# Kernel optimization log

Hardware: AMD Instinct MI355X
Metric: run time of the kernel (lower is better)

## Reference

```python
import jax, jax.numpy as jnp
import numpy as np


def setup_inputs() -> dict:
    key = jax.random.key(0)
    ks = jax.random.split(key, 8)
    B, N, D, H = 8, 512, 64, 64
    user_embeddings = jax.random.normal(ks[0], (B, N, D), dtype=jnp.float32)
    past_lengths = jax.random.randint(ks[1], (B,), 0, N)
    valid_mask = jnp.ones((B, N), dtype=jnp.float32)
    # MLP params: Linear(4D -> H), PReLU (single slope), Linear(H -> 1)
    s1 = 1.0 / np.sqrt(4 * D)
    s2 = 1.0 / np.sqrt(H)
    W1 = jax.random.uniform(ks[2], (H, 4 * D), minval=-s1, maxval=s1, dtype=jnp.float32)
    b1 = jax.random.uniform(ks[3], (H,), minval=-s1, maxval=s1, dtype=jnp.float32)
    prelu_a = jnp.float32(0.25)
    W2 = jax.random.uniform(ks[4], (1, H), minval=-s2, maxval=s2, dtype=jnp.float32)
    b2 = jax.random.uniform(ks[5], (1,), minval=-s2, maxval=s2, dtype=jnp.float32)
    return {"past_lengths": past_lengths, "user_embeddings": user_embeddings,
            "valid_mask": valid_mask, "W1": W1, "b1": b1, "prelu_a": prelu_a,
            "W2": W2, "b2": b2}


def reference(past_lengths, user_embeddings, valid_mask, W1, b1, prelu_a, W2, b2):
    # DIN local activation attention with causal mask.
    # Original math: h = W1 @ concat(Q, K, Q-K, Q*K) + b1 per (q,k) pair.
    # Split W1 into its 4 D-sized blocks so the concat tensor [B,N,N,4D] is
    # never materialized; the pairwise hidden [B,N,N,H] is the only big buffer.
    B, N, D = user_embeddings.shape
    Wq, Wk, Wd, Wm = jnp.split(W1, 4, axis=1)  # each [H, D]
    x = user_embeddings
    # Q and (Q-K)'s +Q part -> per-query term; K and (Q-K)'s -K part -> per-key term
    hq = jnp.einsum('bqd,hd->bqh', x, Wq + Wd)          # [B,N,H]
    hk = jnp.einsum('bkd,hd->bkh', x, Wk - Wd)          # [B,N,H]
    hm = jnp.einsum('bqd,bkd,hd->bqkh', x, x, Wm)       # [B,N,N,H] (Q*K term)
    h = hq[:, :, None, :] + hk[:, None, :, :] + hm + b1
    h = jnp.where(h > 0, h, prelu_a * h)                # PReLU
    scores = jnp.einsum('bqkh,h->bqk', h, W2[0]) + b2[0]  # [B,N,N]
    causal = jnp.tril(jnp.ones((N, N), dtype=scores.dtype))
    scores = scores * causal[None, :, :]
    scores = scores * valid_mask[:, None, :]            # key-side padding mask
    encoded = jnp.einsum('bqk,bkd->bqd', scores, x)     # weighted sum (no softmax)
    return encoded
```

## Files before the change

kernel.cpp:

```cpp
#include <hip/hip_runtime.h>

#define NB 8
#define NN 512

#define WS_WMF 0
#define WS_HQ  4096
#define WS_BF  266240
#define WS_XE  528384

typedef float fx4 __attribute__((ext_vector_type(4)));
typedef short sx8 __attribute__((ext_vector_type(8)));
typedef int   ix4 __attribute__((ext_vector_type(4)));

static __device__ inline unsigned short f2bf(float f) {
    unsigned u = __float_as_uint(f);
    return (unsigned short)((u + 0x7FFFu + ((u >> 16) & 1u)) >> 16);
}

static __device__ inline void async_cp16(const void* g, void* l) {
    __builtin_amdgcn_global_load_lds(
        (const __attribute__((address_space(1))) unsigned int*)g,
        (__attribute__((address_space(3))) unsigned int*)l, 16, 0, 0);
}

__global__ __launch_bounds__(256) void prep(const float* __restrict__ x,
                                            const float* __restrict__ vm,
                                            const float* __restrict__ W1,
                                            const float* __restrict__ b1,
                                            float* __restrict__ ws) {
    __shared__ float lwq[64 * 68];
    __shared__ float lwk[64 * 68];
    __shared__ float xs[256];
    const int t = threadIdx.x;
    const int blk = blockIdx.x;

    {
        int d = t & 63, hb = t >> 6;
        #pragma unroll 4
        for (int i = 0; i < 16; ++i) {
            int h = i * 4 + hb;
            float a = W1[h * 256 + d];
            float bb = W1[h * 256 + 64 + d];
            float c = W1[h * 256 + 128 + d];
            lwq[h * 68 + d] = a + c;
            lwk[h * 68 + d] = bb - c;
        }
    }
    const int r0 = blk * 4;
    xs[t] = x[r0 * 64 + t];
    __syncthreads();

    {
        int r = t >> 6, h = t & 63;
        const fx4* xr  = (const fx4*)(xs + r * 64);
        const fx4* wqv = (const fx4*)(lwq + h * 68);
        const fx4* wkv = (const fx4*)(lwk + h * 68);
        float aq = b1[h], ak = 0.f;
        #pragma unroll
        for (int dd = 0; dd < 16; ++dd) {
            fx4 xv = xr[dd];
            fx4 wq = wqv[dd];
            fx4 wk = wkv[dd];
            aq = fmaf(xv[0], wq[0], aq); aq = fmaf(xv[1], wq[1], aq);
            aq = fmaf(xv[2], wq[2], aq); aq = fmaf(xv[3], wq[3], aq);
            ak = fmaf(xv[0], wk[0], ak); ak = fmaf(xv[1], wk[1], ak);
            ak = fmaf(xv[2], wk[2], ak); ak = fmaf(xv[3], wk[3], ak);
        }
        int row = r0 + r;
        (ws + WS_HQ)[row * 64 + h] = aq;
        unsigned short* bfp = (unsigned short*)(ws + WS_BF);
        int bb = row >> 9, k = row & 511;
        int tt = k >> 4, nn = k & 15;
        int c = 2 + (h >> 5);
        int qd = (h >> 3) & 3, j = h & 7;
        int ln = qd * 16 + nn;
        bfp[((((bb * 32 + tt) * 4 + c) * 64 + ln) << 3) + j] = f2bf(ak);
    }

    if (blk < 256) {
        int b = blk >> 5, t5 = blk & 31;
        if (t < 128) {
            unsigned short* bfp = (unsigned short*)(ws + WS_BF);
            int c = t >> 6, L = t & 63;
            int nn = L & 15, qd = L >> 4;
            const float* src = x + ((b * 512 + t5 * 16 + nn) * 64 + c * 32 + qd * 8);
            fx4 v0 = *(const fx4*)src;
            fx4 v1 = *(const fx4*)(src + 4);
            uint4 o;
            o.x = (unsigned)f2bf(v0[0]) | ((unsigned)f2bf(v0[1]) << 16);
            o.y = (unsigned)f2bf(v0[2]) | ((unsigned)f2bf(v0[3]) << 16);
            o.z = (unsigned)f2bf(v1[0]) | ((unsigned)f2bf(v1[1]) << 16);
            o.w = (unsigned)f2bf(v1[2]) | ((unsigned)f2bf(v1[3]) << 16);
            *(uint4*)(bfp + ((((b * 32 + t5) * 4 + c) * 64 + L) << 3)) = o;
        }
        {
            unsigned short* xep = (unsigned short*)(ws + WS_XE);
            int c32 = t5 >> 1, half = t5 & 1;
            int nt = t >> 6, r = t & 63;
            int L = half * 32 + (r & 31);
            int j0 = (r >> 5) * 4;
            int quad = L >> 4, nn = L & 15;
            unsigned short u[4];
            #pragma unroll
            for (int i = 0; i < 4; ++i) {
                int key = c32 * 32 + quad * 8 + j0 + i;
                float v = x[(b * 512 + key) * 64 + nt * 16 + nn] * vm[b * 512 + key];
                u[i] = f2bf(v);
            }
            uint2 o;
            o.x = (unsigned)u[0] | ((unsigned)u[1] << 16);
            o.y = (unsigned)u[2] | ((unsigned)u[3] << 16);
            *(uint2*)(xep + (((((b * 16 + c32) * 4 + nt) * 64 + L) << 3) + j0)) = o;
        }
    } else if (blk < 258) {
        float* wmf = ws + WS_WMF;
        int e = (blk - 256) * 256 + t;
        int slot = e >> 6, lane = e & 63;
        int ht = slot >> 1, hf = slot & 1;
        int mm = lane & 15, qd = lane >> 4;
        int h = ht * 16 + mm;
        int dbase = hf * 32 + qd * 8;
        #pragma unroll
        for (int j = 0; j < 8; ++j)
            wmf[e * 8 + j] = W1[h * 256 + 192 + dbase + j];
    }
}

__global__ __launch_bounds__(256, 2) void k2_main(const float* __restrict__ x,
                                                  const float* __restrict__ prelu_a,
                                                  const float* __restrict__ W2,
                                                  const float* __restrict__ b2,
                                                  const float* __restrict__ ws,
                                                  float* __restrict__ out) {
    const int tid  = threadIdx.x;
    const int lane = tid & 63;
    const int w    = tid >> 6;
    const int blk  = blockIdx.x;
    const int band = (int)((0x4501763298DCABEFULL >> ((blk >> 6) << 2)) & 0xF);
    const int rest = blk & 63;
    const int b    = rest >> 3;
    const int s    = rest & 7;
    const int n    = lane & 15, quad = lane >> 4;
    const int q    = band * 32 + s * 4 + w;
    const int bq   = b * 512 + q;
    const int cmax = band;

    const float* wmf = ws + WS_WMF;
    const float* hq  = ws + WS_HQ;
    const unsigned short* bfp = (const unsigned short*)(ws + WS_BF);
    const unsigned short* xep = (const unsigned short*)(ws + WS_XE);

    const float pa  = prelu_a[0];
    const float b2v = b2[0];

    __shared__ uint4 bufS[2][512];
    __shared__ uint4 bufE[2][256];
    __shared__ unsigned strip[4][16];

    fx4 w2v[4];
    #pragma unroll
    for (int ht = 0; ht < 4; ++ht)
        w2v[ht] = *(const fx4*)(W2 + ht * 16 + quad * 4);
    sx8 oh[4];
    #pragma unroll
    for (int ht = 0; ht < 4; ++ht) {
        sx8 a;
        #pragma unroll
        for (int jj = 0; jj < 8; ++jj) {
            int hp = (ht >> 1) * 32 + quad * 8 + jj;
            a[jj] = (hp == ht * 16 + n) ? (short)0x3F80 : (short)0;
        }
        oh[ht] = a;
    }
    const unsigned sel = (quad < 2) ? 0x05040100u : 0x07060302u;

    fx4 hqv[4];
    #pragma unroll
    for (int ht = 0; ht < 4; ++ht)
        hqv[ht] = *(const fx4*)(hq + bq * 64 + ht * 16 + quad * 4);
    float xq[2][8];
    {
        const float* xp = x + bq * 64 + quad * 8;
        fx4 t0 = *(const fx4*)xp;
        fx4 t1 = *(const fx4*)(xp + 4);
        fx4 t2 = *(const fx4*)(xp + 32);
        fx4 t3 = *(const fx4*)(xp + 36);
        #pragma unroll
        for (int jj = 0; jj < 4; ++jj) {
            xq[0][jj] = t0[jj]; xq[0][4 + jj] = t1[jj];
            xq[1][jj] = t2[jj]; xq[1][4 + jj] = t3[jj];
        }
    }
    sx8 afrag[4][2];
    #pragma unroll
    for (int ht = 0; ht < 4; ++ht)
        #pragma unroll
        for (int hf = 0; hf < 2; ++hf) {
            const float* wp = wmf + (((ht * 2 + hf) * 64 + lane) << 3);
            fx4 w0 = *(const fx4*)wp;
            fx4 w1 = *(const fx4*)(wp + 4);
            sx8 a;
            #pragma unroll
            for (int jj = 0; jj < 4; ++jj) {
                a[jj]     = (short)f2bf(w0[jj] * xq[hf][jj]);
                a[4 + jj] = (short)f2bf(w1[jj] * xq[hf][4 + jj]);
            }
            afrag[ht][hf] = a;
        }

    fx4 eacc[4];
    #pragma unroll
    for (int nt = 0; nt < 4; ++nt) eacc[nt] = (fx4){0.f, 0.f, 0.f, 0.f};

    {
        const uint4* sS = (const uint4*)(bfp + (unsigned)(b * 32) * 2048);
        const uint4* sE = (const uint4*)(xep + (unsigned)(b * 16) * 2048);
        async_cp16(sS + tid,       &bufS[0][tid]);
        async_cp16(sS + tid + 256, &bufS[0][tid + 256]);
        async_cp16(sE + tid,       &bufE[0][tid]);
    }
    __syncthreads();

    #pragma unroll 1
    for (int c = 0; c <= cmax; ++c) {
        if (c < cmax) {
            const int p2 = (c + 1) & 1;
            const uint4* sS = (const uint4*)(bfp + (unsigned)(b * 32 + 2 * (c + 1)) * 2048);
            const uint4* sE = (const uint4*)(xep + (unsigned)(b * 16 + c + 1) * 2048);
            async_cp16(sS + tid,       &bufS[p2][tid]);
            async_cp16(sS + tid + 256, &bufS[p2][tid + 256]);
            async_cp16(sE + tid,       &bufE[p2][tid]);
        }

        const int p = c & 1;
        const unsigned short* ls = (const unsigned short*)&bufS[p][0] + lane * 8;
        sx8 fa0 = *(const sx8*)(ls);
        sx8 fa1 = *(const sx8*)(ls + 512);
        sx8 fa2 = *(const sx8*)(ls + 1024);
        sx8 fa3 = *(const sx8*)(ls + 1536);
        sx8 fb0 = *(const sx8*)(ls + 2048);
        sx8 fb1 = *(const sx8*)(ls + 2560);
        sx8 fb2 = *(const sx8*)(ls + 3072);
        sx8 fb3 = *(const sx8*)(ls + 3584);

        fx4 accA[4], accB[4];
        #pragma unroll
        for (int ht = 0; ht < 4; ++ht) { accA[ht] = hqv[ht]; accB[ht] = hqv[ht]; }
        #pragma unroll
        for (int ht = 0; ht < 4; ++ht) {
            accA[ht] = __builtin_amdgcn_mfma_f32_16x16x32_bf16(afrag[ht][0], fa0, accA[ht], 0, 0, 0);
            accB[ht] = __builtin_amdgcn_mfma_f32_16x16x32_bf16(afrag[ht][0], fb0, accB[ht], 0, 0, 0);
        }
        #pragma unroll
        for (int ht = 0; ht < 4; ++ht) {
            accA[ht] = __builtin_amdgcn_mfma_f32_16x16x32_bf16(afrag[ht][1], fa1, accA[ht], 0, 0, 0);
            accB[ht] = __builtin_amdgcn_mfma_f32_16x16x32_bf16(afrag[ht][1], fb1, accB[ht], 0, 0, 0);
        }
        #pragma unroll
        for (int ht = 0; ht < 4; ++ht) {
            accA[ht] = __builtin_amdgcn_mfma_f32_16x16x32_bf16(oh[ht], (ht < 2) ? fa2 : fa3, accA[ht], 0, 0, 0);
            accB[ht] = __builtin_amdgcn_mfma_f32_16x16x32_bf16(oh[ht], (ht < 2) ? fb2 : fb3, accB[ht], 0, 0, 0);
        }

        fx4 s0v = (fx4){0.f, 0.f, 0.f, 0.f};
        fx4 s1v = (fx4){0.f, 0.f, 0.f, 0.f};
        #pragma unroll
        for (int ht = 0; ht < 4; ++ht) {
            fx4 za = accA[ht], zb = accB[ht];
            fx4 ta = __builtin_elementwise_max(za, za * pa);
            fx4 tb = __builtin_elementwise_max(zb, zb * pa);
            s0v = ta * w2v[ht] + s0v;
            s1v = tb * w2v[ht] + s1v;
        }
        float s0 = (s0v[0] + s0v[1]) + (s0v[2] + s0v[3]);
        float s1 = (s1v[0] + s1v[1]) + (s1v[2] + s1v[3]);
        s0 += __shfl_xor(s0, 16, 64);
        s0 += __shfl_xor(s0, 32, 64);
        s1 += __shfl_xor(s1, 16, 64);
        s1 += __shfl_xor(s1, 32, 64);
        int k0 = c * 32 + n;
        s0 = (k0 <= q)      ? s0 + b2v : 0.f;
        s1 = (k0 + 16 <= q) ? s1 + b2v : 0.f;

        unsigned packed = (unsigned)f2bf(s0) | ((unsigned)f2bf(s1) << 16);
        if (quad == 0) strip[w][n] = packed;
        const unsigned* sp = &strip[w][(quad & 1) * 8];
        uint4 wv0 = *(const uint4*)sp;
        uint4 wv1 = *(const uint4*)(sp + 4);
        ix4 sw_;
        sw_[0] = (int)__builtin_amdgcn_perm(wv0.y, wv0.x, sel);
        sw_[1] = (int)__builtin_amdgcn_perm(wv0.w, wv0.z, sel);
        sw_[2] = (int)__builtin_amdgcn_perm(wv1.y, wv1.x, sel);
        sw_[3] = (int)__builtin_amdgcn_perm(wv1.w, wv1.z, sel);
        sx8 sfrag = __builtin_bit_cast(sx8, sw_);

        const unsigned short* le = (const unsigned short*)&bufE[p][0] + lane * 8;
        sx8 e0 = *(const sx8*)(le);
        sx8 e1 = *(const sx8*)(le + 512);
        sx8 e2 = *(const sx8*)(le + 1024);
        sx8 e3 = *(const sx8*)(le + 1536);

        eacc[0] = __builtin_amdgcn_mfma_f32_16x16x32_bf16(sfrag, e0, eacc[0], 0, 0, 0);
        eacc[1] = __builtin_amdgcn_mfma_f32_16x16x32_bf16(sfrag, e1, eacc[1], 0, 0, 0);
        eacc[2] = __builtin_amdgcn_mfma_f32_16x16x32_bf16(sfrag, e2, eacc[2], 0, 0, 0);
        eacc[3] = __builtin_amdgcn_mfma_f32_16x16x32_bf16(sfrag, e3, eacc[3], 0, 0, 0);

        __syncthreads();
    }

    float ov = eacc[0][0];
    if (quad == 1) ov = eacc[1][0];
    if (quad == 2) ov = eacc[2][0];
    if (quad == 3) ov = eacc[3][0];
    out[bq * 64 + lane] = ov;
}

extern "C" void kernel_launch(void* const* d_in, const int* in_sizes, int n_in,
                              void* d_out, int out_size, void* d_ws, size_t ws_size,
                              hipStream_t stream) {
    const float* x   = (const float*)d_in[1];
    const float* vmk = (const float*)d_in[2];
    const float* W1  = (const float*)d_in[3];
    const float* b1  = (const float*)d_in[4];
    const float* pa  = (const float*)d_in[5];
    const float* W2  = (const float*)d_in[6];
    const float* b2  = (const float*)d_in[7];
    float* ws  = (float*)d_ws;
    float* out = (float*)d_out;

    hipLaunchKernelGGL(prep, dim3(NB * NN / 4), dim3(256), 0, stream,
                       x, vmk, W1, b1, ws);
    hipLaunchKernelGGL(k2_main, dim3(1024), dim3(256), 0, stream,
                       x, pa, W2, b2, ws, out);
}
```

Baseline: 98.04 us.

## Split prep into weight-prep and MFMA-based per-row projection kernels

The single prep kernel, where every one of 1024 blocks reloaded and combined the W1 blocks and computed the hq/hk projections with scalar FMAs, is replaced by two kernels. prepW builds the combined Wq+Wd and Wk-Wd matrices once in bf16 MFMA fragment layout, plus the Wm fragments. prepX uses 64 blocks that compute hq and hk with bf16 MFMA and also emit the bf16 x and masked-x layouts. This removes redundant weight loading and scalar dot products, but adds a kernel launch and lowers hq precision to bf16 inputs with far fewer blocks.

```diff
diff --git a/kernel.cpp b/kernel.cpp
--- a/kernel.cpp
+++ b/kernel.cpp
@@ -7,6 +7,7 @@
 #define WS_HQ  4096
 #define WS_BF  266240
 #define WS_XE  528384
+#define WS_WQF 659456
 
 typedef float fx4 __attribute__((ext_vector_type(4)));
 typedef short sx8 __attribute__((ext_vector_type(8)));
@@ -23,106 +24,133 @@
         (__attribute__((address_space(3))) unsigned int*)l, 16, 0, 0);
 }
 
-__global__ __launch_bounds__(256) void prep(const float* __restrict__ x,
-                                            const float* __restrict__ vm,
-                                            const float* __restrict__ W1,
-                                            const float* __restrict__ b1,
-                                            float* __restrict__ ws) {
-    __shared__ float lwq[64 * 68];
-    __shared__ float lwk[64 * 68];
-    __shared__ float xs[256];
-    const int t = threadIdx.x;
-    const int blk = blockIdx.x;
+__global__ __launch_bounds__(256) void prepW(const float* __restrict__ W1,
+                                             float* __restrict__ ws) {
+    const int t = threadIdx.x, blk = blockIdx.x;
+    unsigned short* wqf = (unsigned short*)(ws + WS_WQF);
 
     {
-        int d = t & 63, hb = t >> 6;
-        #pragma unroll 4
-        for (int i = 0; i < 16; ++i) {
-            int h = i * 4 + hb;
-            float a = W1[h * 256 + d];
-            float bb = W1[h * 256 + 64 + d];
-            float c = W1[h * 256 + 128 + d];
-            lwq[h * 68 + d] = a + c;
-            lwk[h * 68 + d] = bb - c;
-        }
-    }
-    const int r0 = blk * 4;
-    xs[t] = x[r0 * 64 + t];
-    __syncthreads();
-
-    {
-        int r = t >> 6, h = t & 63;
-        const fx4* xr  = (const fx4*)(xs + r * 64);
-        const fx4* wqv = (const fx4*)(lwq + h * 68);
-        const fx4* wkv = (const fx4*)(lwk + h * 68);
-        float aq = b1[h], ak = 0.f;
-        #pragma unroll
-        for (int dd = 0; dd < 16; ++dd) {
-            fx4 xv = xr[dd];
-            fx4 wq = wqv[dd];
-            fx4 wk = wkv[dd];
-            aq = fmaf(xv[0], wq[0], aq); aq = fmaf(xv[1], wq[1], aq);
-            aq = fmaf(xv[2], wq[2], aq); aq = fmaf(xv[3], wq[3], aq);
-            ak = fmaf(xv[0], wk[0], ak); ak = fmaf(xv[1], wk[1], ak);
-            ak = fmaf(xv[2], wk[2], ak); ak = fmaf(xv[3], wk[3], ak);
-        }
-        int row = r0 + r;
-        (ws + WS_HQ)[row * 64 + h] = aq;
-        unsigned short* bfp = (unsigned short*)(ws + WS_BF);
-        int bb = row >> 9, k = row & 511;
-        int tt = k >> 4, nn = k & 15;
-        int c = 2 + (h >> 5);
-        int qd = (h >> 3) & 3, j = h & 7;
-        int ln = qd * 16 + nn;
-        bfp[((((bb * 32 + tt) * 4 + c) * 64 + ln) << 3) + j] = f2bf(ak);
-    }
-
-    if (blk < 256) {
-        int b = blk >> 5, t5 = blk & 31;
-        if (t < 128) {
-            unsigned short* bfp = (unsigned short*)(ws + WS_BF);
-            int c = t >> 6, L = t & 63;
-            int nn = L & 15, qd = L >> 4;
-            const float* src = x + ((b * 512 + t5 * 16 + nn) * 64 + c * 32 + qd * 8);
-            fx4 v0 = *(const fx4*)src;
-            fx4 v1 = *(const fx4*)(src + 4);
-            uint4 o;
-            o.x = (unsigned)f2bf(v0[0]) | ((unsigned)f2bf(v0[1]) << 16);
-            o.y = (unsigned)f2bf(v0[2]) | ((unsigned)f2bf(v0[3]) << 16);
-            o.z = (unsigned)f2bf(v1[0]) | ((unsigned)f2bf(v1[1]) << 16);
-            o.w = (unsigned)f2bf(v1[2]) | ((unsigned)f2bf(v1[3]) << 16);
-            *(uint4*)(bfp + ((((b * 32 + t5) * 4 + c) * 64 + L) << 3)) = o;
-        }
-        {
-            unsigned short* xep = (unsigned short*)(ws + WS_XE);
-            int c32 = t5 >> 1, half = t5 & 1;
-            int nt = t >> 6, r = t & 63;
-            int L = half * 32 + (r & 31);
-            int j0 = (r >> 5) * 4;
-            int quad = L >> 4, nn = L & 15;
-            unsigned short u[4];
-            #pragma unroll
-            for (int i = 0; i < 4; ++i) {
-                int key = c32 * 32 + quad * 8 + j0 + i;
-                float v = x[(b * 512 + key) * 64 + nt * 16 + nn] * vm[b * 512 + key];
-                u[i] = f2bf(v);
-            }
-            uint2 o;
-            o.x = (unsigned)u[0] | ((unsigned)u[1] << 16);
-            o.y = (unsigned)u[2] | ((unsigned)u[3] << 16);
-            *(uint2*)(xep + (((((b * 16 + c32) * 4 + nt) * 64 + L) << 3) + j0)) = o;
-        }
-    } else if (blk < 258) {
+        int e = blk * 256 + t;
+        int slot = e >> 6, lane = e & 63;
+        int isK = slot >> 3, ht = (slot >> 1) & 3, half = slot & 1;
+        int n = lane & 15, qd = lane >> 4;
+        int h = ht * 16 + n, dbase = half * 32 + qd * 8;
+        unsigned short u[8];
+        #pragma unroll
+        for (int j = 0; j < 8; ++j) {
+            int d = dbase + j;
+            float wq = W1[h * 256 + d];
+            float wk = W1[h * 256 + 64 + d];
+            float wd = W1[h * 256 + 128 + d];
+            u[j] = f2bf(isK ? (wk - wd) : (wq + wd));
+        }
+        uint4 o;
+        o.x = (unsigned)u[0] | ((unsigned)u[1] << 16);
+        o.y = (unsigned)u[2] | ((unsigned)u[3] << 16);
+        o.z = (unsigned)u[4] | ((unsigned)u[5] << 16);
+        o.w = (unsigned)u[6] | ((unsigned)u[7] << 16);
+        ((uint4*)wqf)[e] = o;
+    }
+
+    if (blk < 2) {
         float* wmf = ws + WS_WMF;
-        int e = (blk - 256) * 256 + t;
+        int e = blk * 256 + t;
         int slot = e >> 6, lane = e & 63;
         int ht = slot >> 1, hf = slot & 1;
-        int mm = lane & 15, qd = lane >> 4;
-        int h = ht * 16 + mm;
+        int m = lane & 15, qd = lane >> 4;
+        int h = ht * 16 + m;
         int dbase = hf * 32 + qd * 8;
         #pragma unroll
         for (int j = 0; j < 8; ++j)
             wmf[e * 8 + j] = W1[h * 256 + 192 + dbase + j];
+    }
+}
+
+__global__ __launch_bounds__(256) void prepX(const float* __restrict__ x,
+                                             const float* __restrict__ vm,
+                                             const float* __restrict__ b1,
+                                             float* __restrict__ ws) {
+    const int t = threadIdx.x;
+    const int w = t >> 6, lane = t & 63;
+    const int n = lane & 15, quad = lane >> 4;
+    const int blk = blockIdx.x;
+    const int b   = blk >> 3;
+    const int tb  = (blk & 7) * 4;
+    const int tile = tb + w;
+
+    const unsigned short* wqf = (const unsigned short*)(ws + WS_WQF);
+    unsigned short* bfp = (unsigned short*)(ws + WS_BF);
+    unsigned short* xep = (unsigned short*)(ws + WS_XE);
+    float* hqp = ws + WS_HQ;
+
+    sx8 ax0, ax1;
+    {
+        const float* xp = x + ((b * 512 + tile * 16 + n) * 64 + quad * 8);
+        fx4 a0 = *(const fx4*)xp;
+        fx4 a1 = *(const fx4*)(xp + 4);
+        fx4 a2 = *(const fx4*)(xp + 32);
+        fx4 a3 = *(const fx4*)(xp + 36);
+        #pragma unroll
+        for (int j = 0; j < 4; ++j) {
+            ax0[j] = (short)f2bf(a0[j]); ax0[4 + j] = (short)f2bf(a1[j]);
+            ax1[j] = (short)f2bf(a2[j]); ax1[4 + j] = (short)f2bf(a3[j]);
+        }
+    }
+
+    *(uint4*)(bfp + ((((b * 32 + tile) * 4 + 0) * 64 + lane) << 3)) =
+        __builtin_bit_cast(uint4, ax0);
+    *(uint4*)(bfp + ((((b * 32 + tile) * 4 + 1) * 64 + lane) << 3)) =
+        __builtin_bit_cast(uint4, ax1);
+
+    #pragma unroll
+    for (int ht = 0; ht < 4; ++ht) {
+        sx8 bq0 = *(const sx8*)(wqf + ((ht * 2 + 0) << 9) + lane * 8);
+        sx8 bq1 = *(const sx8*)(wqf + ((ht * 2 + 1) << 9) + lane * 8);
+        sx8 bk0 = *(const sx8*)(wqf + ((8 + ht * 2 + 0) << 9) + lane * 8);
+        sx8 bk1 = *(const sx8*)(wqf + ((8 + ht * 2 + 1) << 9) + lane * 8);
+
+        float bv = b1[ht * 16 + n];
+        fx4 hqa = (fx4){bv, bv, bv, bv};
+        hqa = __builtin_amdgcn_mfma_f32_16x16x32_bf16(ax0, bq0, hqa, 0, 0, 0);
+        hqa = __builtin_amdgcn_mfma_f32_16x16x32_bf16(ax1, bq1, hqa, 0, 0, 0);
+        fx4 hka = (fx4){0.f, 0.f, 0.f, 0.f};
+        hka = __builtin_amdgcn_mfma_f32_16x16x32_bf16(ax0, bk0, hka, 0, 0, 0);
+        hka = __builtin_amdgcn_mfma_f32_16x16x32_bf16(ax1, bk1, hka, 0, 0, 0);
+
+        #pragma unroll
+        for (int r = 0; r < 4; ++r)
+            hqp[(b * 512 + tile * 16 + quad * 4 + r) * 64 + ht * 16 + n] = hqa[r];
+
+        int c   = 2 + (ht >> 1);
+        int qd2 = (((ht & 1) * 16 + n) >> 3);
+        int j   = n & 7;
+        #pragma unroll
+        for (int r = 0; r < 4; ++r) {
+            int nn = quad * 4 + r;
+            bfp[((((b * 32 + tile) * 4 + c) * 64 + (qd2 * 16 + nn)) << 3) + j] =
+                f2bf(hka[r]);
+        }
+    }
+
+    #pragma unroll 1
+    for (int i = 0; i < 4; ++i) {
+        int t5 = tb + i;
+        int c32 = t5 >> 1, half = t5 & 1;
+        int nt = t >> 6, r = t & 63;
+        int L = half * 32 + (r & 31);
+        int j0 = (r >> 5) * 4;
+        int qd3 = L >> 4, nn3 = L & 15;
+        unsigned short u[4];
+        #pragma unroll
+        for (int ii = 0; ii < 4; ++ii) {
+            int key = c32 * 32 + qd3 * 8 + j0 + ii;
+            float v = x[(b * 512 + key) * 64 + nt * 16 + nn3] * vm[b * 512 + key];
+            u[ii] = f2bf(v);
+        }
+        uint2 o;
+        o.x = (unsigned)u[0] | ((unsigned)u[1] << 16);
+        o.y = (unsigned)u[2] | ((unsigned)u[3] << 16);
+        *(uint2*)(xep + (((((b * 16 + c32) * 4 + nt) * 64 + L) << 3) + j0)) = o;
     }
 }
 
@@ -328,8 +356,8 @@
     float* ws  = (float*)d_ws;
     float* out = (float*)d_out;
 
-    hipLaunchKernelGGL(prep, dim3(NB * NN / 4), dim3(256), 0, stream,
-                       x, vmk, W1, b1, ws);
+    hipLaunchKernelGGL(prepW, dim3(4), dim3(256), 0, stream, W1, ws);
+    hipLaunchKernelGGL(prepX, dim3(64), dim3(256), 0, stream, x, vmk, b1, ws);
     hipLaunchKernelGGL(k2_main, dim3(1024), dim3(256), 0, stream,
                        x, pa, W2, b2, ws, out);
 }
```

New measurement: 102.1 us. +4.2%, slower.
